# Performance work log

Hardware: AMD Instinct MI355X
Metric: run time of the kernel (lower is better)

The kernel has to match this reference:

```python
import jax, jax.numpy as jnp
import numpy as np

B, T, H = 32, 2000, 512      # batch, encoder frames, d_model
L = 256                      # max label length (padded output tokens)
THRESHOLD = 0.95


def setup_inputs() -> dict:
    key = jax.random.key(0)
    k1, k2, k3 = jax.random.split(key, 3)
    hidden = jax.random.normal(k1, (B, T, H), dtype=jnp.float32)
    alphas = jax.random.uniform(k2, (B, T), dtype=jnp.float32)
    target_lengths = jax.random.randint(k3, (B,), 64, L + 1)
    return {"hidden": hidden, "alphas": alphas, "target_lengths": target_lengths}


def _cif(hidden, alphas):
    # Continuous integrate-and-fire scan over time.
    Bt, Tt, Ht = hidden.shape

    def step(carry, xs):
        integrate, frame = carry          # [B], [B,H]
        alpha, h = xs                     # [B], [B,H]
        dist_completion = 1.0 - integrate
        integrate = integrate + alpha
        fire = integrate >= THRESHOLD     # [B] bool
        cur = jnp.where(fire, dist_completion, alpha)
        remainds = alpha - cur
        frame_out = frame + cur[:, None] * h
        integ_next = jnp.where(fire, integrate - 1.0, integrate)
        frame_next = jnp.where(fire[:, None], remainds[:, None] * h, frame_out)
        return (integ_next, frame_next), (frame_out, fire)

    init = (jnp.zeros((Bt,), hidden.dtype), jnp.zeros((Bt, Ht), hidden.dtype))
    _, (frames, fires) = jax.lax.scan(step, init, (alphas.T, jnp.swapaxes(hidden, 0, 1)))
    frames = jnp.swapaxes(frames, 0, 1)   # [B,T,H] accumulated frame at each step
    fires = fires.T                        # [B,T] fire events

    # Gather fired frames into padded [B, L, H] token tensor (vectorized scatter).
    tok = jnp.cumsum(fires.astype(jnp.int32), axis=1) - 1   # token index per fired frame
    valid = fires & (tok >= 0) & (tok < L)
    out = jnp.zeros((Bt, L, Ht), hidden.dtype)
    b_idx = jnp.arange(Bt)[:, None]
    out = out.at[b_idx, jnp.clip(tok, 0, L - 1)].add(
        frames * valid[..., None].astype(hidden.dtype))
    return out


def reference(hidden, alphas, target_lengths):
    # Rescale alphas so each row sums to target length (noise term omitted).
    num = target_lengths.astype(alphas.dtype)
    alphas = alphas * (num / alphas.sum(-1))[:, None]
    return _cif(hidden, alphas)
```

## Files before the change

### kernel.cpp

```cpp
#include <hip/hip_runtime.h>

#define BB 32
#define TT 2000
#define NG 500
#define HH 512
#define LL 256
#define THRESH 0.95f


__global__ __launch_bounds__(256) void cif_scan_kernel(
    const float* __restrict__ alphas, const int* __restrict__ tlen,
    float* __restrict__ cur_g, int* __restrict__ fire_pos,
    int* __restrict__ nfires, float* __restrict__ scale_g)
{
    const int b = blockIdx.x;
    const int tid = threadIdx.x;
    __shared__ float sa[TT];
    __shared__ float scur[TT];
    __shared__ double red[256];
    __shared__ int fp_s[LL];
    __shared__ float s_scale;
    __shared__ int s_nf;

    const float4* a4 = (const float4*)(alphas + b * TT);
    float4* sa4 = (float4*)sa;
    double s = 0.0;
    for (int g = tid; g < NG; g += 256) {
        float4 v = a4[g];
        sa4[g] = v;
        s += (double)v.x + (double)v.y + (double)v.z + (double)v.w;
    }
    red[tid] = s;
    __syncthreads();
    for (int off = 128; off > 0; off >>= 1) {
        if (tid < off) red[tid] += red[tid + off];
        __syncthreads();
    }
    if (tid == 0) {
        const float sumf = (float)red[0];
        const float sc = (float)tlen[b] / sumf;
        s_scale = sc;
        scale_g[b] = sc;
    }
    __syncthreads();
    const float sc = s_scale;

    for (int g = tid; g < NG; g += 256) {
        float4 v = sa4[g];
        v.x *= sc; v.y *= sc; v.z *= sc; v.w *= sc;
        sa4[g] = v;
    }
    __syncthreads();

    if (tid == 0) {
        float integ = 0.0f;
        int nf = 0;
        const float4* s4 = (const float4*)sa;
        float4* c4 = (float4*)scur;
        float4 buf[4];
        #pragma unroll
        for (int i = 0; i < 4; ++i) buf[i] = s4[i];
        for (int blk = 0; blk < 125; ++blk) {
            #pragma unroll
            for (int i = 0; i < 4; ++i) {
                const int g = blk * 4 + i;
                const float4 c = buf[i];
                if (g + 4 < NG) buf[i] = s4[g + 4];
                const float av[4] = {c.x, c.y, c.z, c.w};
                float ov[4];
                #pragma unroll
                for (int j = 0; j < 4; ++j) {
                    const float a = av[j];
                    float ii = integ + a;
                    float o = a;
                    if (ii >= THRESH) {
                        o = 1.0f - integ;
                        ii -= 1.0f;
                        if (nf < LL) fp_s[nf] = g * 4 + j;
                        nf++;
                    }
                    ov[j] = o;
                    integ = ii;
                }
                c4[g] = make_float4(ov[0], ov[1], ov[2], ov[3]);
            }
        }
        s_nf = (nf < LL) ? nf : LL;
    }
    __syncthreads();

    const int nf = s_nf;
    if (tid == 0) nfires[b] = nf;
    float4* cg4 = (float4*)(cur_g + b * TT);
    const float4* sc4 = (const float4*)scur;
    for (int g = tid; g < NG; g += 256) cg4[g] = sc4[g];
    if (tid < LL) fire_pos[b * LL + tid] = (tid < nf) ? fp_s[tid] : 0;
}

__global__ __launch_bounds__(128) void cif_gather_kernel(
    const float* __restrict__ hidden, const float* __restrict__ alphas,
    const float* __restrict__ cur_g, const float* __restrict__ scale_g,
    const int* __restrict__ fire_pos, const int* __restrict__ nfires,
    float* __restrict__ out)
{
    const int l = blockIdx.x;
    const int b = blockIdx.y;
    const int tid = threadIdx.x;

    float4 acc = make_float4(0.f, 0.f, 0.f, 0.f);
    const int F = nfires[b];
    if (l < F) {
        const int e = fire_pos[b * LL + l];
        const float* hb = hidden + (size_t)b * TT * HH + (size_t)tid * 4;
        const float* wb = cur_g + b * TT;
        int t0 = 0;
        if (l > 0) {
            const int sp = fire_pos[b * LL + l - 1];
            const float a_sp = alphas[b * TT + sp] * scale_g[b];
            const float rem = a_sp - wb[sp];
            const float4 hv = *(const float4*)(hb + (size_t)sp * HH);
            acc.x = rem * hv.x; acc.y = rem * hv.y;
            acc.z = rem * hv.z; acc.w = rem * hv.w;
            t0 = sp + 1;
        }
        int t = t0;
        float w0 = wb[t];
        float4 h0 = *(const float4*)(hb + (size_t)t * HH);
        if (t < e) {
            float w1 = wb[t + 1];
            float4 h1 = *(const float4*)(hb + (size_t)(t + 1) * HH);
            while (t + 2 <= e) {
                const float w2 = wb[t + 2];
                const float4 h2 = *(const float4*)(hb + (size_t)(t + 2) * HH);
                acc.x += w0 * h0.x; acc.y += w0 * h0.y;
                acc.z += w0 * h0.z; acc.w += w0 * h0.w;
                w0 = w1; h0 = h1; w1 = w2; h1 = h2; ++t;
            }
            acc.x += w0 * h0.x; acc.y += w0 * h0.y;
            acc.z += w0 * h0.z; acc.w += w0 * h0.w;
            w0 = w1; h0 = h1;
        }
        acc.x += w0 * h0.x; acc.y += w0 * h0.y;
        acc.z += w0 * h0.z; acc.w += w0 * h0.w;
    }
    *(float4*)(out + ((size_t)b * LL + l) * HH + (size_t)tid * 4) = acc;
}

extern "C" void kernel_launch(void* const* d_in, const int* in_sizes, int n_in,
                              void* d_out, int out_size, void* d_ws, size_t ws_size,
                              hipStream_t stream) {
    const float* hidden = (const float*)d_in[0];
    const float* alphas = (const float*)d_in[1];
    const int*   tlen   = (const int*)d_in[2];
    float* out = (float*)d_out;

    float* cur_g    = (float*)d_ws;
    int*   fire_pos = (int*)(cur_g + BB * TT);
    int*   nfires   = fire_pos + BB * LL;
    float* scale_g  = (float*)(nfires + BB);

    cif_scan_kernel<<<BB, 256, 0, stream>>>(alphas, tlen, cur_g, fire_pos,
                                            nfires, scale_g);
    cif_gather_kernel<<<dim3(LL, BB), 128, 0, stream>>>(hidden, alphas, cur_g,
                                                        scale_g, fire_pos,
                                                        nfires, out);
}
```

Baseline: 263.1 us.

## Make serial scan branchless with fire bitmasks and compact fire records

```diff
diff --git a/kernel.cpp b/kernel.cpp
--- a/kernel.cpp
+++ b/kernel.cpp
@@ -3,6 +3,7 @@
 #define BB 32
 #define TT 2000
 #define NG 500
+#define NW 63
 #define HH 512
 #define LL 256
 #define THRESH 0.95f
@@ -10,17 +11,17 @@
 
 __global__ __launch_bounds__(256) void cif_scan_kernel(
     const float* __restrict__ alphas, const int* __restrict__ tlen,
-    float* __restrict__ cur_g, int* __restrict__ fire_pos,
-    int* __restrict__ nfires, float* __restrict__ scale_g)
+    int2* __restrict__ rec, int* __restrict__ nfires,
+    float* __restrict__ scale_g)
 {
     const int b = blockIdx.x;
     const int tid = threadIdx.x;
     __shared__ float sa[TT];
-    __shared__ float scur[TT];
+    __shared__ float sinteg[TT];
     __shared__ double red[256];
-    __shared__ int fp_s[LL];
+    __shared__ unsigned smask[NW];
+    __shared__ int spre[NW + 1];
     __shared__ float s_scale;
-    __shared__ int s_nf;
 
     const float4* a4 = (const float4*)(alphas + b * TT);
     float4* sa4 = (float4*)sa;
@@ -53,55 +54,89 @@
     __syncthreads();
 
     if (tid == 0) {
+        const float4* s4 = (const float4*)sa;
+        float4* ip4 = (float4*)sinteg;
         float integ = 0.0f;
-        int nf = 0;
-        const float4* s4 = (const float4*)sa;
-        float4* c4 = (float4*)scur;
-        float4 buf[4];
+        unsigned mask = 0;
+        float4 buf[8];
         #pragma unroll
-        for (int i = 0; i < 4; ++i) buf[i] = s4[i];
-        for (int blk = 0; blk < 125; ++blk) {
+        for (int i = 0; i < 8; ++i) buf[i] = s4[i];
+
+        for (int w = 0; w < 62; ++w) {
             #pragma unroll
-            for (int i = 0; i < 4; ++i) {
-                const int g = blk * 4 + i;
+            for (int i = 0; i < 8; ++i) {
+                const int g = w * 8 + i;
                 const float4 c = buf[i];
-                if (g + 4 < NG) buf[i] = s4[g + 4];
+                if (g + 8 < NG) buf[i] = s4[g + 8];
                 const float av[4] = {c.x, c.y, c.z, c.w};
-                float ov[4];
+                float iv[4];
                 #pragma unroll
                 for (int j = 0; j < 4; ++j) {
                     const float a = av[j];
                     float ii = integ + a;
-                    float o = a;
-                    if (ii >= THRESH) {
-                        o = 1.0f - integ;
-                        ii -= 1.0f;
-                        if (nf < LL) fp_s[nf] = g * 4 + j;
-                        nf++;
-                    }
-                    ov[j] = o;
+                    const bool fire = (ii >= THRESH);
+                    const float iim1 = ii - 1.0f;
+                    ii = fire ? iim1 : ii;
+                    mask |= fire ? (1u << (i * 4 + j)) : 0u;
+                    iv[j] = ii;
                     integ = ii;
                 }
-                c4[g] = make_float4(ov[0], ov[1], ov[2], ov[3]);
-            }
-        }
-        s_nf = (nf < LL) ? nf : LL;
-    }
-    __syncthreads();
-
-    const int nf = s_nf;
-    if (tid == 0) nfires[b] = nf;
-    float4* cg4 = (float4*)(cur_g + b * TT);
-    const float4* sc4 = (const float4*)scur;
-    for (int g = tid; g < NG; g += 256) cg4[g] = sc4[g];
-    if (tid < LL) fire_pos[b * LL + tid] = (tid < nf) ? fp_s[tid] : 0;
+                ip4[g] = make_float4(iv[0], iv[1], iv[2], iv[3]);
+            }
+            smask[w] = mask;
+            mask = 0;
+        }
+        #pragma unroll
+        for (int i = 0; i < 4; ++i) {
+            const int g = 496 + i;
+            const float4 c = buf[i];
+            const float av[4] = {c.x, c.y, c.z, c.w};
+            float iv[4];
+            #pragma unroll
+            for (int j = 0; j < 4; ++j) {
+                const float a = av[j];
+                float ii = integ + a;
+                const bool fire = (ii >= THRESH);
+                const float iim1 = ii - 1.0f;
+                ii = fire ? iim1 : ii;
+                mask |= fire ? (1u << (i * 4 + j)) : 0u;
+                iv[j] = ii;
+                integ = ii;
+            }
+            ip4[g] = make_float4(iv[0], iv[1], iv[2], iv[3]);
+        }
+        smask[62] = mask;
+    }
+    __syncthreads();
+
+    if (tid == 0) {
+        int r = 0;
+        for (int w = 0; w < NW; ++w) { spre[w] = r; r += __popc(smask[w]); }
+        spre[NW] = r;
+        nfires[b] = (r < LL) ? r : LL;
+    }
+    __syncthreads();
+    if (tid < NW) {
+        unsigned m = smask[tid];
+        int tok = spre[tid];
+        while (m) {
+            const int j = __ffs(m) - 1;
+            m &= m - 1;
+            const int t = tid * 32 + j;
+            if (tok < LL) {
+                const float dist = (t == 0) ? 1.0f : (1.0f - sinteg[t - 1]);
+                int2 r; r.x = t; r.y = __float_as_int(dist);
+                rec[b * LL + tok] = r;
+            }
+            ++tok;
+        }
+    }
 }
 
 __global__ __launch_bounds__(128) void cif_gather_kernel(
     const float* __restrict__ hidden, const float* __restrict__ alphas,
-    const float* __restrict__ cur_g, const float* __restrict__ scale_g,
-    const int* __restrict__ fire_pos, const int* __restrict__ nfires,
-    float* __restrict__ out)
+    const float* __restrict__ scale_g, const int2* __restrict__ rec,
+    const int* __restrict__ nfires, float* __restrict__ out)
 {
     const int l = blockIdx.x;
     const int b = blockIdx.y;
@@ -110,27 +145,31 @@
     float4 acc = make_float4(0.f, 0.f, 0.f, 0.f);
     const int F = nfires[b];
     if (l < F) {
-        const int e = fire_pos[b * LL + l];
+        const int2 re = rec[b * LL + l];
+        const int e = re.x;
+        const float dist = __int_as_float(re.y);
+        const float sc = scale_g[b];
         const float* hb = hidden + (size_t)b * TT * HH + (size_t)tid * 4;
-        const float* wb = cur_g + b * TT;
+        const float* ab = alphas + b * TT;
         int t0 = 0;
         if (l > 0) {
-            const int sp = fire_pos[b * LL + l - 1];
-            const float a_sp = alphas[b * TT + sp] * scale_g[b];
-            const float rem = a_sp - wb[sp];
+            const int2 rp = rec[b * LL + l - 1];
+            const int sp = rp.x;
+            const float dp = __int_as_float(rp.y);
+            const float rem = ab[sp] * sc - dp;
             const float4 hv = *(const float4*)(hb + (size_t)sp * HH);
             acc.x = rem * hv.x; acc.y = rem * hv.y;
             acc.z = rem * hv.z; acc.w = rem * hv.w;
             t0 = sp + 1;
         }
         int t = t0;
-        float w0 = wb[t];
+        float w0 = (t < e) ? ab[t] * sc : dist;
         float4 h0 = *(const float4*)(hb + (size_t)t * HH);
         if (t < e) {
-            float w1 = wb[t + 1];
+            float w1 = (t + 1 < e) ? ab[t + 1] * sc : dist;
             float4 h1 = *(const float4*)(hb + (size_t)(t + 1) * HH);
             while (t + 2 <= e) {
-                const float w2 = wb[t + 2];
+                const float w2 = (t + 2 < e) ? ab[t + 2] * sc : dist;
                 const float4 h2 = *(const float4*)(hb + (size_t)(t + 2) * HH);
                 acc.x += w0 * h0.x; acc.y += w0 * h0.y;
                 acc.z += w0 * h0.z; acc.w += w0 * h0.w;
@@ -154,14 +193,11 @@
     const int*   tlen   = (const int*)d_in[2];
     float* out = (float*)d_out;
 
-    float* cur_g    = (float*)d_ws;
-    int*   fire_pos = (int*)(cur_g + BB * TT);
-    int*   nfires   = fire_pos + BB * LL;
-    float* scale_g  = (float*)(nfires + BB);
-
-    cif_scan_kernel<<<BB, 256, 0, stream>>>(alphas, tlen, cur_g, fire_pos,
-                                            nfires, scale_g);
-    cif_gather_kernel<<<dim3(LL, BB), 128, 0, stream>>>(hidden, alphas, cur_g,
-                                                        scale_g, fire_pos,
-                                                        nfires, out);
+    int2*  rec     = (int2*)d_ws;
+    int*   nfires  = (int*)(rec + BB * LL);
+    float* scale_g = (float*)(nfires + BB);
+
+    cif_scan_kernel<<<BB, 256, 0, stream>>>(alphas, tlen, rec, nfires, scale_g);
+    cif_gather_kernel<<<dim3(LL, BB), 128, 0, stream>>>(hidden, alphas, scale_g,
+                                                        rec, nfires, out);
 }
```

Measured after the change: 264.6 us. Within noise of the previous version (+0.6%).
